# Performance work log

Hardware: AMD Instinct MI355X
Metric: run time of the kernel (lower is better)

Reference implementation:

```python
import jax, jax.numpy as jnp
import numpy as np

N = 12                      # matrix size (input_size)
TRI = N * (N + 1) // 2      # 78 lower-triangular entries
HID = 512
BATCH = 262144


def setup_inputs() -> dict:
    key = jax.random.key(0)
    ks = jax.random.split(key, 4)
    s1 = 1.0 / np.sqrt(N)
    s2 = 1.0 / np.sqrt(HID)
    return {
        "x": jax.random.normal(ks[0], (BATCH, N), dtype=jnp.float32),
        "W1": jax.random.normal(ks[1], (N, HID), dtype=jnp.float32) * s1,
        "b1": jnp.zeros((HID,), dtype=jnp.float32),
        "W2": jax.random.normal(ks[2], (HID, HID), dtype=jnp.float32) * s2,
        "b2": jnp.zeros((HID,), dtype=jnp.float32),
        "W3": jax.random.normal(ks[3], (HID, TRI + 1), dtype=jnp.float32) * s2,
        "b3": jnp.zeros((TRI + 1,), dtype=jnp.float32),
    }


def reference(x, W1, b1, W2, b2, W3, b3):
    # 3-layer MLP (assumed parent-class structure): relu, relu, softplus
    h = jax.nn.relu(x @ W1 + b1)
    h = jax.nn.relu(h @ W2 + b2)
    out = jax.nn.softplus(h @ W3 + b3)          # [B, TRI+1]
    # Vectorized row-major lower-triangular scatter (replaces nested python loop)
    rows, cols = jnp.tril_indices(N)            # row-major order matches idx loop
    B = x.shape[0]
    L = jnp.zeros((B, N, N), dtype=out.dtype).at[:, rows, cols].set(out[:, :TRI])
    MMT = jnp.einsum('bij,bkj->bik', L, L)      # M @ M^T, PSD [B, N, N]
    c = out[:, TRI]                             # [B]
    return MMT, c
```

## Files before the change

kernel.cpp:

```cpp
#include <hip/hip_runtime.h>
#include <math.h>

typedef __attribute__((ext_vector_type(8))) _Float16 fp16x8;
typedef __attribute__((ext_vector_type(4))) _Float16 fp16x4;
typedef __attribute__((ext_vector_type(2))) __fp16 hfp16x2;
typedef __attribute__((ext_vector_type(4))) __fp16 hfp16x4;
typedef __attribute__((ext_vector_type(4))) float floatx4;

#define HID 512
#define TRIC 78
#define OUTC 79
#define BATCH 262144
#define HPAD 520
#define LPAD 88
#define XPAD 24
#define X_OFF 33280

#define W2P_OFF 16384
#define W3P_OFF 278528

__global__ __launch_bounds__(256) void prep_kernel(const float* __restrict__ W1,
                                                   const float* __restrict__ W2,
                                                   const float* __restrict__ W3,
                                                   _Float16* __restrict__ wsh) {
  int g = blockIdx.x * 256 + threadIdx.x;
  int lane = g & 63;
  int l15 = lane & 15, q = lane >> 4;
  fp16x8 v;
  if (g < 2048) {
    int ct = g >> 6;
    int c = ct * 16 + l15;
#pragma unroll
    for (int j = 0; j < 8; ++j) {
      int k = q * 8 + j;
      v[j] = (k < 12) ? (_Float16)W1[k * HID + c] : (_Float16)0.f;
    }
    *(fp16x8*)(wsh + (size_t)g * 8) = v;
  } else if (g < 34816) {
    int h = g - 2048;
    int fk = h >> 6;
    int kb = fk & 15, ct = fk >> 4;
    int c = ct * 16 + l15;
    int kbase = kb * 32 + q * 8;
#pragma unroll
    for (int j = 0; j < 8; ++j) v[j] = (_Float16)W2[(kbase + j) * HID + c];
    *(fp16x8*)(wsh + W2P_OFF + (size_t)h * 8) = v;
  } else if (g < 39936) {
    int h = g - 34816;
    int fk = h >> 6;
    int kb = fk & 15, ct = fk >> 4;
    int c = ct * 16 + l15;
    int kbase = kb * 32 + q * 8;
#pragma unroll
    for (int j = 0; j < 8; ++j)
      v[j] = (c < OUTC) ? (_Float16)W3[(kbase + j) * OUTC + c] : (_Float16)0.f;
    *(fp16x8*)(wsh + W3P_OFF + (size_t)h * 8) = v;
  }
}

__device__ __forceinline__ float softplus_f(float v) {
  float e = __expf(-fabsf(v));
  return fmaxf(v, 0.f) + __logf(1.f + e);
}

__device__ __forceinline__ fp16x4 relu_pk4(floatx4 a) {
  hfp16x2 lo = __builtin_amdgcn_cvt_pkrtz(fmaxf(a[0], 0.f), fmaxf(a[1], 0.f));
  hfp16x2 hi = __builtin_amdgcn_cvt_pkrtz(fmaxf(a[2], 0.f), fmaxf(a[3], 0.f));
  hfp16x4 r = __builtin_shufflevector(lo, hi, 0, 1, 2, 3);
  return __builtin_bit_cast(fp16x4, r);
}

__device__ __forceinline__ fp16x4 pk4(floatx4 a) {
  hfp16x2 lo = __builtin_amdgcn_cvt_pkrtz(a[0], a[1]);
  hfp16x2 hi = __builtin_amdgcn_cvt_pkrtz(a[2], a[3]);
  hfp16x4 r = __builtin_shufflevector(lo, hi, 0, 1, 2, 3);
  return __builtin_bit_cast(fp16x4, r);
}

__global__ __launch_bounds__(512, 4) void fused_kernel(const float* __restrict__ x,
                                                       const float* __restrict__ b1,
                                                       const float* __restrict__ b2,
                                                       const float* __restrict__ b3,
                                                       const _Float16* __restrict__ wsh,
                                                       float* __restrict__ out) {
  __shared__ __align__(16) _Float16 hbuf[X_OFF + 64 * XPAD];
  const int tid = threadIdx.x;
  const int wave = tid >> 6, lane = tid & 63;
  const int l15 = lane & 15, quad = lane >> 4;
  const int r0 = blockIdx.x * 64;

  const fp16x8* w1p = (const fp16x8*)wsh;
  const fp16x8* w2p = (const fp16x8*)(wsh + W2P_OFF);
  const fp16x8* w3p = (const fp16x8*)(wsh + W3P_OFF);

  {
    _Float16* xs = hbuf + X_OFF;
    const float* xg = x + (size_t)r0 * 12;
    if (tid < 256) {
      int e = 512 + tid;
      int row = e / 12, col = e - row * 12;
      xs[row * XPAD + col] = (_Float16)xg[e];
      xs[(tid >> 2) * XPAD + 12 + (tid & 3)] = (_Float16)0.f;
    }
    {
      int row = tid / 12, col = tid - row * 12;
      xs[row * XPAD + col] = (_Float16)xg[tid];
    }
  }
  fp16x8 a1p[4];
#pragma unroll
  for (int ct = 0; ct < 4; ++ct) a1p[ct] = w1p[(wave * 4 + ct) * 64 + lane];
  __syncthreads();

  fp16x8 zf;
#pragma unroll
  for (int j = 0; j < 8; ++j) zf[j] = (_Float16)0.f;

  floatx4 bq[4];
#pragma unroll
  for (int ct = 0; ct < 4; ++ct)
    bq[ct] = *(const floatx4*)(b1 + wave * 64 + ct * 16 + quad * 4);

  floatx4 acc[4][4];
#pragma unroll
  for (int ct = 0; ct < 4; ++ct)
#pragma unroll
    for (int nt = 0; nt < 4; ++nt) acc[ct][nt] = bq[ct];

  {
    const _Float16* xs = hbuf + X_OFF;
    fp16x8 xb[4];
#pragma unroll
    for (int nt = 0; nt < 4; ++nt)
      xb[nt] = (quad < 2) ? *(const fp16x8*)(xs + (nt * 16 + l15) * XPAD + quad * 8) : zf;
#pragma unroll
    for (int ct = 0; ct < 4; ++ct) {
#pragma unroll
      for (int nt = 0; nt < 4; ++nt)
        acc[ct][nt] = __builtin_amdgcn_mfma_f32_16x16x32_f16(a1p[ct], xb[nt], acc[ct][nt], 0, 0, 0);
    }
  }

#pragma unroll
  for (int ct = 0; ct < 4; ++ct)
#pragma unroll
    for (int nt = 0; nt < 4; ++nt)
      *(fp16x4*)(hbuf + (nt * 16 + l15) * HPAD + wave * 64 + ct * 16 + quad * 4) =
          relu_pk4(acc[ct][nt]);
  fp16x8 ap[4];
#pragma unroll
  for (int ct = 0; ct < 4; ++ct) ap[ct] = w2p[((wave * 4 + ct) * 16 + 0) * 64 + lane];
  __syncthreads();

#pragma unroll
  for (int ct = 0; ct < 4; ++ct)
    bq[ct] = *(const floatx4*)(b2 + wave * 64 + ct * 16 + quad * 4);
#pragma unroll
  for (int ct = 0; ct < 4; ++ct)
#pragma unroll
    for (int nt = 0; nt < 4; ++nt) acc[ct][nt] = bq[ct];

#pragma unroll 2
  for (int kb = 0; kb < 16; ++kb) {
    fp16x8 a[4], b[4];
#pragma unroll
    for (int ct = 0; ct < 4; ++ct) a[ct] = ap[ct];
#pragma unroll
    for (int nt = 0; nt < 4; ++nt)
      b[nt] = *(const fp16x8*)(hbuf + (nt * 16 + l15) * HPAD + kb * 32 + quad * 8);
    const int kbn = (kb + 1) & 15;
#pragma unroll
    for (int ct = 0; ct < 4; ++ct) ap[ct] = w2p[((wave * 4 + ct) * 16 + kbn) * 64 + lane];
    __builtin_amdgcn_s_setprio(1);
#pragma unroll
    for (int ct = 0; ct < 4; ++ct)
#pragma unroll
      for (int nt = 0; nt < 4; ++nt)
        acc[ct][nt] = __builtin_amdgcn_mfma_f32_16x16x32_f16(a[ct], b[nt], acc[ct][nt], 0, 0, 0);
    __builtin_amdgcn_s_setprio(0);
  }

  __syncthreads();

#pragma unroll
  for (int ct = 0; ct < 4; ++ct)
#pragma unroll
    for (int nt = 0; nt < 4; ++nt)
      *(fp16x4*)(hbuf + (nt * 16 + l15) * HPAD + wave * 64 + ct * 16 + quad * 4) =
          relu_pk4(acc[ct][nt]);

  const int mt3 = wave >> 1;
  const int codd = wave & 1;
  const int c0 = codd ? 3 : 0;
  const int nct = codd ? 2 : 3;

  floatx4 b3q[3];
#pragma unroll
  for (int j = 0; j < 3; ++j) {
#pragma unroll
    for (int r = 0; r < 4; ++r) {
      int c = (c0 + j) * 16 + quad * 4 + r;
      b3q[j][r] = (j < nct && c < OUTC) ? b3[c] : 0.f;
    }
  }
  floatx4 acc3[3];
#pragma unroll
  for (int j = 0; j < 3; ++j) acc3[j] = b3q[j];

  fp16x8 ap3[3];
#pragma unroll
  for (int j = 0; j < 3; ++j) ap3[j] = zf;
#pragma unroll
  for (int j = 0; j < 3; ++j)
    if (j < nct) ap3[j] = w3p[((c0 + j) * 16 + 0) * 64 + lane];
  __syncthreads();

  fp16x8 bp3 = *(const fp16x8*)(hbuf + (mt3 * 16 + l15) * HPAD + 0 * 32 + quad * 8);
#pragma unroll 2
  for (int kb = 0; kb < 16; ++kb) {
    fp16x8 bfrag = bp3;
    fp16x8 a3[3];
#pragma unroll
    for (int j = 0; j < 3; ++j) a3[j] = ap3[j];
    const int kbn = (kb + 1) & 15;
    bp3 = *(const fp16x8*)(hbuf + (mt3 * 16 + l15) * HPAD + kbn * 32 + quad * 8);
#pragma unroll
    for (int j = 0; j < 3; ++j)
      if (j < nct) ap3[j] = w3p[((c0 + j) * 16 + kbn) * 64 + lane];
    __builtin_amdgcn_s_setprio(1);
#pragma unroll
    for (int j = 0; j < 3; ++j)
      if (j < nct)
        acc3[j] = __builtin_amdgcn_mfma_f32_16x16x32_f16(a3[j], bfrag, acc3[j], 0, 0, 0);
    __builtin_amdgcn_s_setprio(0);
  }
  __syncthreads();

#pragma unroll
  for (int j = 0; j < 3; ++j)
    if (j < nct) {
      floatx4 v;
#pragma unroll
      for (int r = 0; r < 4; ++r) v[r] = softplus_f(acc3[j][r]);
      *(fp16x4*)(hbuf + (mt3 * 16 + l15) * LPAD + (c0 + j) * 16 + quad * 4) = pk4(v);
    }
  if (codd && quad == 3)
    out[(size_t)BATCH * 144 + r0 + mt3 * 16 + l15] = softplus_f(acc3[1][2]);
  __syncthreads();

  {
    const int rowl = tid >> 3;
    const int sub = tid & 7;
    const _Float16* Lr = hbuf + rowl * LPAD;

    float R[80];
#pragma unroll
    for (int q = 0; q < 10; ++q) {
      fp16x8 v = *(const fp16x8*)(Lr + q * 8);
#pragma unroll
      for (int r = 0; r < 8; ++r) R[q * 8 + r] = (float)v[r];
    }

    float Lj0[12], Lj1[12];
    {
      const int tj = (sub * (sub + 1)) >> 1;
#pragma unroll
      for (int k = 0; k < 12; ++k) Lj0[k] = (k <= sub) ? (float)Lr[tj + k] : 0.f;
#pragma unroll
      for (int k = 0; k < 12; ++k) Lj1[k] = 0.f;
      const int j1 = sub + 8;
      if (sub < 4) {
        const int tj1 = (j1 * (j1 + 1)) >> 1;
#pragma unroll
        for (int k = 0; k < 12; ++k) Lj1[k] = (k <= j1) ? (float)Lr[tj1 + k] : 0.f;
      }
    }

    float* Mg = out + ((size_t)r0 + rowl) * 144;
#pragma unroll
    for (int i = 0; i < 12; ++i) {
      const int ti = (i * (i + 1)) >> 1;
      float s0 = 0.f, s1 = 0.f;
#pragma unroll
      for (int k = 0; k <= i; ++k) {
        const float li = R[ti + k];
        s0 = fmaf(li, Lj0[k], s0);
        s1 = fmaf(li, Lj1[k], s1);
      }
      Mg[i * 12 + sub] = s0;
      if (sub < 4) Mg[i * 12 + sub + 8] = s1;
    }
  }
}

extern "C" void kernel_launch(void* const* d_in, const int* in_sizes, int n_in,
                              void* d_out, int out_size, void* d_ws, size_t ws_size,
                              hipStream_t stream) {
  const float* x  = (const float*)d_in[0];
  const float* W1 = (const float*)d_in[1];
  const float* b1 = (const float*)d_in[2];
  const float* W2 = (const float*)d_in[3];
  const float* b2 = (const float*)d_in[4];
  const float* W3 = (const float*)d_in[5];
  const float* b3 = (const float*)d_in[6];
  float* out = (float*)d_out;
  _Float16* wsh = (_Float16*)d_ws;

  prep_kernel<<<156, 256, 0, stream>>>(W1, W2, W3, wsh);
  fused_kernel<<<BATCH / 64, 512, 0, stream>>>(x, b1, b2, b3, wsh, out);
}
```

Baseline: 332.0 us.

## Reassign MMT epilogue: one lane per row, waves split symmetric column pairs

The L·Lᵀ epilogue used to give each batch row to 8 threads, each holding the full 80-entry L row in registers. Now each lane owns one batch row and each of six waves computes a balanced pair of columns (j, 11-j). Only the lower triangle is computed, and each value is mirrored to both symmetric output positions, which removes the duplicate dot products. The cost is that waves 6-7 sit idle in this phase, and the per-lane global stores are strided by 144 floats, which hurts coalescing.

Measured after the change: 375.2 us. 13.0% more time.

```diff
diff --git a/kernel.cpp b/kernel.cpp
--- a/kernel.cpp
+++ b/kernel.cpp
@@ -249,47 +249,41 @@
   __syncthreads();
 
   {
-    const int rowl = tid >> 3;
-    const int sub = tid & 7;
-    const _Float16* Lr = hbuf + rowl * LPAD;
-
-    float R[80];
-#pragma unroll
-    for (int q = 0; q < 10; ++q) {
-      fp16x8 v = *(const fp16x8*)(Lr + q * 8);
-#pragma unroll
-      for (int r = 0; r < 8; ++r) R[q * 8 + r] = (float)v[r];
-    }
-
-    float Lj0[12], Lj1[12];
-    {
-      const int tj = (sub * (sub + 1)) >> 1;
-#pragma unroll
-      for (int k = 0; k < 12; ++k) Lj0[k] = (k <= sub) ? (float)Lr[tj + k] : 0.f;
-#pragma unroll
-      for (int k = 0; k < 12; ++k) Lj1[k] = 0.f;
-      const int j1 = sub + 8;
-      if (sub < 4) {
-        const int tj1 = (j1 * (j1 + 1)) >> 1;
-#pragma unroll
-        for (int k = 0; k < 12; ++k) Lj1[k] = (k <= j1) ? (float)Lr[tj1 + k] : 0.f;
-      }
-    }
-
-    float* Mg = out + ((size_t)r0 + rowl) * 144;
-#pragma unroll
-    for (int i = 0; i < 12; ++i) {
-      const int ti = (i * (i + 1)) >> 1;
-      float s0 = 0.f, s1 = 0.f;
-#pragma unroll
-      for (int k = 0; k <= i; ++k) {
-        const float li = R[ti + k];
-        s0 = fmaf(li, Lj0[k], s0);
-        s1 = fmaf(li, Lj1[k], s1);
-      }
-      Mg[i * 12 + sub] = s0;
-      if (sub < 4) Mg[i * 12 + sub + 8] = s1;
-    }
+    const _Float16* Lr = hbuf + lane * LPAD;
+    float* Mg = out + ((size_t)r0 + lane) * 144;
+
+#define TRI_(j) (((j) * ((j) + 1)) >> 1)
+#define MMT_ARM(JA, JB, NQ)                                                  \
+  {                                                                          \
+    float R[(NQ) * 8];                                                       \
+    _Pragma("unroll") for (int q = 0; q < (NQ); ++q) {                       \
+      fp16x8 v = *(const fp16x8*)(Lr + q * 8);                               \
+      _Pragma("unroll") for (int r = 0; r < 8; ++r) R[q * 8 + r] = (float)v[r]; \
+    }                                                                        \
+    _Pragma("unroll") for (int i = 0; i <= (JA); ++i) {                      \
+      float s = 0.f;                                                         \
+      _Pragma("unroll") for (int k = 0; k <= i; ++k)                         \
+        s = fmaf(R[TRI_(i) + k], R[TRI_(JA) + k], s);                        \
+      Mg[i * 12 + (JA)] = s;                                                 \
+      if (i < (JA)) Mg[(JA) * 12 + i] = s;                                   \
+    }                                                                        \
+    _Pragma("unroll") for (int i = 0; i <= (JB); ++i) {                      \
+      float s = 0.f;                                                         \
+      _Pragma("unroll") for (int k = 0; k <= i; ++k)                         \
+        s = fmaf(R[TRI_(i) + k], R[TRI_(JB) + k], s);                        \
+      Mg[i * 12 + (JB)] = s;                                                 \
+      if (i < (JB)) Mg[(JB) * 12 + i] = s;                                   \
+    }                                                                        \
+  }
+
+    if (wave == 0)      MMT_ARM(11, 0, 10)
+    else if (wave == 1) MMT_ARM(10, 1, 9)
+    else if (wave == 2) MMT_ARM(9, 2, 7)
+    else if (wave == 3) MMT_ARM(8, 3, 6)
+    else if (wave == 4) MMT_ARM(7, 4, 5)
+    else if (wave == 5) MMT_ARM(6, 5, 4)
+#undef MMT_ARM
+#undef TRI_
   }
 }
 
```
